# Kernel tuning notes

Measured on AMD Instinct MI355X. Metric: run time of the kernel, lower is better.

## Reference

```python
import jax, jax.numpy as jnp
import numpy as np

N_HEADS, N_LEVELS, N_POINTS = 8, 4, 4


def _bilinear(im, grid, H, W):
    # im: [N, D, H*W] flattened level feature, grid: [N, Q, P, 2] in [-1, 1]
    # F.grid_sample bilinear, padding_mode='zeros', align_corners=False
    N, Q, P, _ = grid.shape
    D = im.shape[1]
    gx = ((grid[..., 0] + 1.0) * W - 1.0) * 0.5
    gy = ((grid[..., 1] + 1.0) * H - 1.0) * 0.5
    x0f = jnp.floor(gx)
    y0f = jnp.floor(gy)
    x0 = x0f.astype(jnp.int32)
    y0 = y0f.astype(jnp.int32)
    wx1 = gx - x0f
    wy1 = gy - y0f
    acc = jnp.zeros((N, D, Q * P), im.dtype)
    corners = ((0, 0, (1 - wx1) * (1 - wy1)), (1, 0, wx1 * (1 - wy1)),
               (0, 1, (1 - wx1) * wy1), (1, 1, wx1 * wy1))
    for dx, dy, wgt in corners:
        xi = x0 + dx
        yi = y0 + dy
        valid = (xi >= 0) & (xi < W) & (yi >= 0) & (yi < H)
        idx = jnp.clip(yi, 0, H - 1) * W + jnp.clip(xi, 0, W - 1)
        v = jnp.take_along_axis(im, idx.reshape(N, 1, Q * P), axis=2)  # [N,D,QP]
        acc = acc + v * jnp.where(valid, wgt, 0.0).reshape(N, 1, Q * P)
    return acc.reshape(N, D, Q, P)


def _forward(query, value, reference_points, shapes_np,
             w_off, b_off, w_attn, b_attn, w_val, b_val, w_out, b_out):
    B, Q, E = query.shape
    H_, L, P = N_HEADS, N_LEVELS, N_POINTS
    D = E // H_
    v = (value @ w_val + b_val).reshape(B, -1, H_, D)  # [B, Nv, H, D]
    off = (query @ w_off + b_off).reshape(B, Q, H_, L, P, 2)
    attn = (query @ w_attn + b_attn).reshape(B, Q, H_, L * P)
    attn = jax.nn.softmax(attn, axis=-1).reshape(B, Q, H_, L, P)
    # offset_scale = [W_l, H_l] per level
    scale = jnp.asarray(np.stack([shapes_np[:, 1], shapes_np[:, 0]], -1), jnp.float32)
    locs = reference_points[:, :, None, :, None, :] + off / scale[None, None, None, :, None, :]
    grid = 2.0 * locs - 1.0  # [B, Q, H, L, P, 2]
    starts = np.concatenate([[0], np.cumsum(shapes_np[:, 0] * shapes_np[:, 1])]).astype(int)
    out = jnp.zeros((B * H_, D, Q), query.dtype)
    for lvl in range(L):
        h, w = int(shapes_np[lvl, 0]), int(shapes_np[lvl, 1])
        feat = v[:, starts[lvl]:starts[lvl + 1]]                      # [B, h*w, H, D]
        feat = feat.transpose(0, 2, 3, 1).reshape(B * H_, D, h * w)   # [BH, D, hw]
        g = jnp.transpose(grid[:, :, :, lvl], (0, 2, 1, 3, 4)).reshape(B * H_, Q, P, 2)
        sampled = _bilinear(feat, g, h, w)                            # [BH, D, Q, P]
        wl = jnp.transpose(attn[:, :, :, lvl], (0, 2, 1, 3)).reshape(B * H_, 1, Q, P)
        out = out + (sampled * wl).sum(-1)                            # [BH, D, Q]
    out = out.reshape(B, H_ * D, Q).transpose(0, 2, 1)                # [B, Q, E]
    return out @ w_out + b_out


def setup_inputs() -> dict:
    key = jax.random.key(0)
    ks = jax.random.split(key, 12)
    B, Q, E = 2, 19947, 256
    L, H_, P = N_LEVELS, N_HEADS, N_POINTS
    shapes = jnp.array([[100, 150], [50, 75], [25, 38], [13, 19]], dtype=jnp.int64)
    s = 0.02
    return {
        'query': jax.random.normal(ks[0], (B, Q, E), jnp.float32),
        'value': jax.random.normal(ks[1], (B, Q, E), jnp.float32),
        'reference_points': jax.random.uniform(ks[2], (B, Q, L, 2), jnp.float32),
        'spatial_shapes': shapes,
        'w_off': jax.random.normal(ks[3], (E, H_ * L * P * 2), jnp.float32) * s,
        'b_off': jax.random.normal(ks[4], (H_ * L * P * 2,), jnp.float32) * s,
        'w_attn': jax.random.normal(ks[5], (E, H_ * L * P), jnp.float32) * s,
        'b_attn': jax.random.normal(ks[6], (H_ * L * P,), jnp.float32) * s,
        'w_val': jax.random.normal(ks[7], (E, E), jnp.float32) * s,
        'b_val': jax.random.normal(ks[8], (E,), jnp.float32) * s,
        'w_out': jax.random.normal(ks[9], (E, E), jnp.float32) * s,
        'b_out': jax.random.normal(ks[10], (E,), jnp.float32) * s,
    }


def reference(query, value, reference_points, spatial_shapes,
              w_off, b_off, w_attn, b_attn, w_val, b_val, w_out, b_out):
    shapes_np = np.asarray(spatial_shapes)
    return _forward(query, value, reference_points, shapes_np,
                    w_off, b_off, w_attn, b_attn, w_val, b_val, w_out, b_out)
```

## Files before the change

kernel.cpp:

```cpp
#include <hip/hip_runtime.h>
#include <math.h>

#define B_    2
#define Q_    19947
#define E_    256
#define H_    8
#define D_    32
#define L_    4
#define P_    4

typedef _Float16 f16_t;
typedef f16_t f16x8 __attribute__((ext_vector_type(8)));
typedef f16_t f16x4 __attribute__((ext_vector_type(4)));
typedef float f32x4 __attribute__((ext_vector_type(4)));

__global__ __launch_bounds__(256)
void transpose_all(const float* __restrict__ w_val, const float* __restrict__ w_off,
                   const float* __restrict__ w_attn, const float* __restrict__ w_out,
                   f16_t* __restrict__ WtV, f16_t* __restrict__ WtQ,
                   f16_t* __restrict__ WtO)
{
    const float* in; f16_t* out; int N;
    switch (blockIdx.z) {
        case 0:  in = w_val;  out = WtV;             N = 256; break;
        case 1:  in = w_off;  out = WtQ;             N = 256; break;
        case 2:  in = w_attn; out = WtQ + 256 * 256; N = 128; break;
        default: in = w_out;  out = WtO;             N = 256; break;
    }
    const int nt = blockIdx.x * 32;
    if (nt >= N) return;
    const int kt = blockIdx.y * 32;

    __shared__ float tile[32][33];
    const int x  = threadIdx.x & 31;
    const int y0 = threadIdx.x >> 5;
    #pragma unroll
    for (int p = 0; p < 4; ++p)
        tile[y0 + p * 8][x] = in[(size_t)(kt + y0 + p * 8) * N + nt + x];
    __syncthreads();
    #pragma unroll
    for (int p = 0; p < 4; ++p)
        out[(size_t)(nt + y0 + p * 8) * 256 + kt + x] = (f16_t)tile[x][y0 + p * 8];
}

__global__ __launch_bounds__(256, 5)
void gemm_proj(const float* __restrict__ Aval, const float* __restrict__ Aqry,
               const f16_t* __restrict__ WtV, const f16_t* __restrict__ WtQ,
               const float* __restrict__ b_val, const float* __restrict__ b_off,
               const float* __restrict__ b_attn,
               f16_t* __restrict__ v_proj, float* __restrict__ off_b,
               float* __restrict__ attn_b, int M)
{
    constexpr int K = 256, BK = 32, NIT = K / BK;
    __shared__ __align__(16) f16_t As[2][64][40];
    __shared__ __align__(16) f16_t Bs[2][128][40];

    const int t    = threadIdx.x;
    const int m0   = blockIdx.x * 64;
    const int by   = blockIdx.y;
    const bool isVal = (by < 2);
    const float*  Af = isVal ? Aval : Aqry;
    const f16_t*  Wt = isVal ? WtV : WtQ;
    const int n0     = isVal ? by * 128 : (by - 2) * 128;

    const int lane = t & 63;
    const int w    = t >> 6;
    const int wm   = w & 1, wn = w >> 1;
    const int quad = lane >> 4, l16 = lane & 15;

    const int srow = t >> 2;
    const int skc  = (t & 3) * 8;

    f32x4 acc[2][4];
    #pragma unroll
    for (int i = 0; i < 2; ++i)
        #pragma unroll
        for (int j = 0; j < 4; ++j) {
            f32x4 z = {0.f, 0.f, 0.f, 0.f};
            acc[i][j] = z;
        }

    f16x8 aval;
    uint4 bval0, bval1;

    auto load_stage = [&](int k0) {
        const int gm = m0 + srow;
        if (gm < M) {
            const float4 v0 = *(const float4*)(Af + (size_t)gm * 256 + k0 + skc);
            const float4 v1 = *(const float4*)(Af + (size_t)gm * 256 + k0 + skc + 4);
            aval[0] = (f16_t)v0.x; aval[1] = (f16_t)v0.y;
            aval[2] = (f16_t)v0.z; aval[3] = (f16_t)v0.w;
            aval[4] = (f16_t)v1.x; aval[5] = (f16_t)v1.y;
            aval[6] = (f16_t)v1.z; aval[7] = (f16_t)v1.w;
        } else {
            #pragma unroll
            for (int i = 0; i < 8; ++i) aval[i] = (f16_t)0.f;
        }
        bval0 = *(const uint4*)(Wt + (size_t)(n0 + srow)      * 256 + k0 + skc);
        bval1 = *(const uint4*)(Wt + (size_t)(n0 + srow + 64) * 256 + k0 + skc);
    };
    auto store_stage = [&](int buf) {
        *(f16x8*)&As[buf][srow][skc]      = aval;
        *(uint4*)&Bs[buf][srow][skc]      = bval0;
        *(uint4*)&Bs[buf][srow + 64][skc] = bval1;
    };

    load_stage(0);
    store_stage(0);
    int cur = 0;

    #pragma unroll
    for (int it = 0; it < NIT; ++it) {
        __syncthreads();
        if (it + 1 < NIT)
            load_stage((it + 1) * BK);

        f16x8 af[2], bfr[4];
        #pragma unroll
        for (int i = 0; i < 2; ++i)
            af[i] = *(const f16x8*)&As[cur][wm * 32 + i * 16 + l16][quad * 8];
        #pragma unroll
        for (int j = 0; j < 4; ++j)
            bfr[j] = *(const f16x8*)&Bs[cur][wn * 64 + j * 16 + l16][quad * 8];
        #pragma unroll
        for (int i = 0; i < 2; ++i)
            #pragma unroll
            for (int j = 0; j < 4; ++j)
                acc[i][j] = __builtin_amdgcn_mfma_f32_16x16x32_f16(af[i], bfr[j], acc[i][j], 0, 0, 0);

        if (it + 1 < NIT)
            store_stage(cur ^ 1);
        cur ^= 1;
    }

    #pragma unroll
    for (int j = 0; j < 4; ++j) {
        const int gn = n0 + wn * 64 + j * 16 + l16;
        const float bv = isVal ? b_val[gn] : (gn < 256 ? b_off[gn] : b_attn[gn - 256]);
        #pragma unroll
        for (int i = 0; i < 2; ++i) {
            #pragma unroll
            for (int r = 0; r < 4; ++r) {
                const int gm = m0 + wm * 32 + i * 16 + quad * 4 + r;
                if (gm < M) {
                    const float val = acc[i][j][r] + bv;
                    if (isVal)
                        v_proj[(size_t)gm * 256 + gn] = (f16_t)val;
                    else if (gn < 256)
                        off_b[(size_t)gm * 256 + gn] = val;
                    else
                        attn_b[(size_t)gm * 128 + (gn - 256)] = val;
                }
            }
        }
    }
}

__global__ __launch_bounds__(256, 4)
void msda_fused(const f16_t* __restrict__ v,
                const float* __restrict__ off,
                const float* __restrict__ attn,
                const float* __restrict__ ref,
                const f16_t* __restrict__ WoT,
                const float* __restrict__ b_out,
                float* __restrict__ out,
                int BQ)
{
    constexpr int SH[4] = {100, 50, 25, 13};
    constexpr int SW[4] = {150, 75, 38, 19};
    constexpr int ST[4] = {0, 15000, 18750, 19700};

    __shared__ __align__(16) f16_t Samp[16][264];

    const int t   = threadIdx.x;
    const int bq0 = blockIdx.x * 16;

    #pragma unroll
    for (int r = 0; r < 2; ++r) {
        const int g    = t >> 2;
        const int qi   = (g >> 3) + r * 8;
        const int h    = g & 7;
        const int lane = t & 3;
        const int bq   = bq0 + qi;

        float acc[8] = {0.f, 0.f, 0.f, 0.f, 0.f, 0.f, 0.f, 0.f};

        if (bq < BQ) {
            const int b = bq / Q_;
            const f16_t* vbase = v + ((size_t)b * Q_) * E_ + h * D_ + lane * 8;
            const float* offp  = off  + (size_t)bq * 256 + h * 32;
            const float* attnp = attn + (size_t)bq * 128 + h * 16;

            float aw[16];
            #pragma unroll
            for (int i = 0; i < 4; ++i) {
                const float4 x = *(const float4*)(attnp + i * 4);
                aw[i*4+0] = x.x; aw[i*4+1] = x.y; aw[i*4+2] = x.z; aw[i*4+3] = x.w;
            }
            float mx = aw[0];
            #pragma unroll
            for (int i = 1; i < 16; ++i) mx = fmaxf(mx, aw[i]);
            float sum = 0.f;
            #pragma unroll
            for (int i = 0; i < 16; ++i) { aw[i] = expf(aw[i] - mx); sum += aw[i]; }
            const float inv = 1.f / sum;
            #pragma unroll
            for (int i = 0; i < 16; ++i) aw[i] *= inv;

            const float4 r01 = *(const float4*)(ref + (size_t)bq * 8);
            const float4 r23 = *(const float4*)(ref + (size_t)bq * 8 + 4);
            const float rx[4] = {r01.x, r01.z, r23.x, r23.z};
            const float ry[4] = {r01.y, r01.w, r23.y, r23.w};

            #pragma unroll
            for (int l = 0; l < L_; ++l) {
                const float fW = (float)SW[l], fH = (float)SH[l];
                const int   Ww = SW[l], Hh = SH[l], st = ST[l];
                #pragma unroll
                for (int pp = 0; pp < 2; ++pp) {
                    const float4 o2 = *(const float4*)(offp + l * 8 + pp * 4);
                    #pragma unroll
                    for (int q = 0; q < 2; ++q) {
                        const int   p  = pp * 2 + q;
                        const float ox = q ? o2.z : o2.x;
                        const float oy = q ? o2.w : o2.y;
                        const float wA = aw[l * 4 + p];
                        const float gx = fmaf(rx[l], fW, ox) - 0.5f;
                        const float gy = fmaf(ry[l], fH, oy) - 0.5f;
                        const float x0f = floorf(gx), y0f = floorf(gy);
                        const int   x0  = (int)x0f,   y0  = (int)y0f;
                        const float wx1 = gx - x0f,   wy1 = gy - y0f;
                        const float wx0 = 1.f - wx1,  wy0 = 1.f - wy1;

                        const float mxw0 = ((unsigned)x0     < (unsigned)Ww) ? wx0 : 0.f;
                        const float mxw1 = ((unsigned)(x0+1) < (unsigned)Ww) ? wx1 : 0.f;
                        const float myw0 = ((unsigned)y0     < (unsigned)Hh) ? wy0 : 0.f;
                        const float myw1 = ((unsigned)(y0+1) < (unsigned)Hh) ? wy1 : 0.f;
                        const int xc0 = min(max(x0, 0),     Ww - 1);
                        const int xc1 = min(max(x0 + 1, 0), Ww - 1);
                        const int yc0 = min(max(y0, 0),     Hh - 1);
                        const int yc1 = min(max(y0 + 1, 0), Hh - 1);

                        const float w00 = wA * mxw0 * myw0;
                        const float w10 = wA * mxw1 * myw0;
                        const float w01 = wA * mxw0 * myw1;
                        const float w11 = wA * mxw1 * myw1;

                        const f16x8 s00 = *(const f16x8*)(vbase + (size_t)(st + yc0 * Ww + xc0) * E_);
                        const f16x8 s10 = *(const f16x8*)(vbase + (size_t)(st + yc0 * Ww + xc1) * E_);
                        const f16x8 s01 = *(const f16x8*)(vbase + (size_t)(st + yc1 * Ww + xc0) * E_);
                        const f16x8 s11 = *(const f16x8*)(vbase + (size_t)(st + yc1 * Ww + xc1) * E_);

                        #pragma unroll
                        for (int c = 0; c < 8; ++c) {
                            acc[c] = fmaf(w00, (float)s00[c], acc[c]);
                            acc[c] = fmaf(w10, (float)s10[c], acc[c]);
                            acc[c] = fmaf(w01, (float)s01[c], acc[c]);
                            acc[c] = fmaf(w11, (float)s11[c], acc[c]);
                        }
                    }
                }
            }
        }

        f16x8 o;
        #pragma unroll
        for (int c = 0; c < 8; ++c) o[c] = (f16_t)acc[c];
        *(f16x8*)&Samp[qi][h * 32 + lane * 8] = o;
    }

    __syncthreads();

    const int lane = t & 63;
    const int w    = t >> 6;
    const int quad = lane >> 4, l16 = lane & 15;

    f16x8 af[8];
    #pragma unroll
    for (int kf = 0; kf < 8; ++kf)
        af[kf] = *(const f16x8*)&Samp[l16][kf * 32 + quad * 8];

    f32x4 acc4[4];
    #pragma unroll
    for (int j = 0; j < 4; ++j) {
        f32x4 z = {0.f, 0.f, 0.f, 0.f};
        acc4[j] = z;
    }

    #pragma unroll
    for (int j = 0; j < 4; ++j) {
        const int n = w * 64 + j * 16 + l16;
        const f16_t* bp = WoT + (size_t)n * 256 + quad * 8;
        #pragma unroll
        for (int kf = 0; kf < 8; ++kf) {
            const f16x8 bfr = *(const f16x8*)(bp + kf * 32);
            acc4[j] = __builtin_amdgcn_mfma_f32_16x16x32_f16(af[kf], bfr, acc4[j], 0, 0, 0);
        }
    }

    #pragma unroll
    for (int j = 0; j < 4; ++j) {
        const int n  = w * 64 + j * 16 + l16;
        const float bv = b_out[n];
        #pragma unroll
        for (int r = 0; r < 4; ++r) {
            const int gm = bq0 + quad * 4 + r;
            if (gm < BQ)
                out[(size_t)gm * 256 + n] = acc4[j][r] + bv;
        }
    }
}

extern "C" void kernel_launch(void* const* d_in, const int* in_sizes, int n_in,
                              void* d_out, int out_size, void* d_ws, size_t ws_size,
                              hipStream_t stream)
{
    const float* query  = (const float*)d_in[0];
    const float* value  = (const float*)d_in[1];
    const float* refpts = (const float*)d_in[2];
    const float* w_off  = (const float*)d_in[4];
    const float* b_off  = (const float*)d_in[5];
    const float* w_attn = (const float*)d_in[6];
    const float* b_attn = (const float*)d_in[7];
    const float* w_val  = (const float*)d_in[8];
    const float* b_val  = (const float*)d_in[9];
    const float* w_out  = (const float*)d_in[10];
    const float* b_out  = (const float*)d_in[11];
    float* out = (float*)d_out;

    const int BQ = B_ * Q_;

    char* ws = (char*)d_ws;
    f16_t* v_proj = (f16_t*)ws;                       ws += (size_t)BQ * 256 * 2;
    float* off_b  = (float*)ws;                       ws += (size_t)BQ * 256 * 4;
    float* attn_b = (float*)ws;                       ws += (size_t)BQ * 128 * 4;
    f16_t* WtV    = (f16_t*)ws;                       ws += (size_t)256 * 256 * 2;
    f16_t* WtQ    = (f16_t*)ws;                       ws += (size_t)384 * 256 * 2;
    f16_t* WtO    = (f16_t*)ws;

    const dim3 blk(256);

    transpose_all<<<dim3(8, 8, 4), blk, 0, stream>>>(w_val, w_off, w_attn, w_out,
                                                     WtV, WtQ, WtO);

    const int mg = (BQ + 63) / 64;

    gemm_proj<<<dim3(mg, 5), blk, 0, stream>>>(
        value, query, WtV, WtQ, b_val, b_off, b_attn,
        v_proj, off_b, attn_b, BQ);

    msda_fused<<<dim3((BQ + 15) / 16), blk, 0, stream>>>(
        v_proj, off_b, attn_b, refpts, WtO, b_out, out, BQ);
}
```

Measured before the change: 297.2 us.

## Replace LDS-staged projection GEMM with direct-to-register MFMA operand loads

```diff
diff --git a/kernel.cpp b/kernel.cpp
--- a/kernel.cpp
+++ b/kernel.cpp
@@ -43,33 +43,37 @@
         out[(size_t)(nt + y0 + p * 8) * 256 + kt + x] = (f16_t)tile[x][y0 + p * 8];
 }
 
-__global__ __launch_bounds__(256, 5)
-void gemm_proj(const float* __restrict__ Aval, const float* __restrict__ Aqry,
-               const f16_t* __restrict__ WtV, const f16_t* __restrict__ WtQ,
-               const float* __restrict__ b_val, const float* __restrict__ b_off,
-               const float* __restrict__ b_attn,
-               f16_t* __restrict__ v_proj, float* __restrict__ off_b,
-               float* __restrict__ attn_b, int M)
+__global__ __launch_bounds__(256)
+void gemm_direct(const float* __restrict__ value, const float* __restrict__ query,
+                 const f16_t* __restrict__ WtV, const f16_t* __restrict__ WtQ,
+                 const float* __restrict__ b_val, const float* __restrict__ b_off,
+                 const float* __restrict__ b_attn,
+                 f16_t* __restrict__ v_proj, float* __restrict__ off_b,
+                 float* __restrict__ attn_b, int M)
 {
-    constexpr int K = 256, BK = 32, NIT = K / BK;
-    __shared__ __align__(16) f16_t As[2][64][40];
-    __shared__ __align__(16) f16_t Bs[2][128][40];
-
     const int t    = threadIdx.x;
-    const int m0   = blockIdx.x * 64;
-    const int by   = blockIdx.y;
-    const bool isVal = (by < 2);
-    const float*  Af = isVal ? Aval : Aqry;
-    const f16_t*  Wt = isVal ? WtV : WtQ;
-    const int n0     = isVal ? by * 128 : (by - 2) * 128;
-
+    const int w    = t >> 6;
     const int lane = t & 63;
-    const int w    = t >> 6;
-    const int wm   = w & 1, wn = w >> 1;
     const int quad = lane >> 4, l16 = lane & 15;
 
-    const int srow = t >> 2;
-    const int skc  = (t & 3) * 8;
+    const int by     = blockIdx.y;
+    const bool isVal = (by < 4);
+    const float* A   = isVal ? value : query;
+    const f16_t* Wt  = isVal ? WtV : WtQ;
+    const int n0     = isVal ? by * 64 : (by - 4) * 64;
+
+    const int mb = blockIdx.x * 128 + w * 32;
+
+    const float* aptr[2];
+    #pragma unroll
+    for (int i = 0; i < 2; ++i) {
+        const int gm = min(mb + i * 16 + l16, M - 1);
+        aptr[i] = A + (size_t)gm * 256 + quad * 8;
+    }
+    const f16_t* bptr[4];
+    #pragma unroll
+    for (int j = 0; j < 4; ++j)
+        bptr[j] = Wt + (size_t)(n0 + j * 16 + l16) * 256 + quad * 8;
 
     f32x4 acc[2][4];
     #pragma unroll
@@ -80,68 +84,68 @@
             acc[i][j] = z;
         }
 
-    f16x8 aval;
-    uint4 bval0, bval1;
-
-    auto load_stage = [&](int k0) {
-        const int gm = m0 + srow;
-        if (gm < M) {
-            const float4 v0 = *(const float4*)(Af + (size_t)gm * 256 + k0 + skc);
-            const float4 v1 = *(const float4*)(Af + (size_t)gm * 256 + k0 + skc + 4);
-            aval[0] = (f16_t)v0.x; aval[1] = (f16_t)v0.y;
-            aval[2] = (f16_t)v0.z; aval[3] = (f16_t)v0.w;
-            aval[4] = (f16_t)v1.x; aval[5] = (f16_t)v1.y;
-            aval[6] = (f16_t)v1.z; aval[7] = (f16_t)v1.w;
-        } else {
-            #pragma unroll
-            for (int i = 0; i < 8; ++i) aval[i] = (f16_t)0.f;
-        }
-        bval0 = *(const uint4*)(Wt + (size_t)(n0 + srow)      * 256 + k0 + skc);
-        bval1 = *(const uint4*)(Wt + (size_t)(n0 + srow + 64) * 256 + k0 + skc);
-    };
-    auto store_stage = [&](int buf) {
-        *(f16x8*)&As[buf][srow][skc]      = aval;
-        *(uint4*)&Bs[buf][srow][skc]      = bval0;
-        *(uint4*)&Bs[buf][srow + 64][skc] = bval1;
-    };
-
-    load_stage(0);
-    store_stage(0);
-    int cur = 0;
-
-    #pragma unroll
-    for (int it = 0; it < NIT; ++it) {
-        __syncthreads();
-        if (it + 1 < NIT)
-            load_stage((it + 1) * BK);
-
-        f16x8 af[2], bfr[4];
+    float4 acur[2][2], anxt[2][2];
+    uint4  bcur[4],    bnxt[4];
+
+    #pragma unroll
+    for (int i = 0; i < 2; ++i) {
+        acur[i][0] = *(const float4*)(aptr[i]);
+        acur[i][1] = *(const float4*)(aptr[i] + 4);
+    }
+    #pragma unroll
+    for (int j = 0; j < 4; ++j)
+        bcur[j] = *(const uint4*)(bptr[j]);
+
+    #pragma unroll
+    for (int it = 0; it < 8; ++it) {
+        if (it < 7) {
+            const int k1 = (it + 1) * 32;
+            #pragma unroll
+            for (int i = 0; i < 2; ++i) {
+                anxt[i][0] = *(const float4*)(aptr[i] + k1);
+                anxt[i][1] = *(const float4*)(aptr[i] + k1 + 4);
+            }
+            #pragma unroll
+            for (int j = 0; j < 4; ++j)
+                bnxt[j] = *(const uint4*)(bptr[j] + k1);
+        }
+
+        f16x8 af[2];
+        #pragma unroll
+        for (int i = 0; i < 2; ++i) {
+            af[i][0] = (f16_t)acur[i][0].x; af[i][1] = (f16_t)acur[i][0].y;
+            af[i][2] = (f16_t)acur[i][0].z; af[i][3] = (f16_t)acur[i][0].w;
+            af[i][4] = (f16_t)acur[i][1].x; af[i][5] = (f16_t)acur[i][1].y;
+            af[i][6] = (f16_t)acur[i][1].z; af[i][7] = (f16_t)acur[i][1].w;
+        }
         #pragma unroll
         for (int i = 0; i < 2; ++i)
-            af[i] = *(const f16x8*)&As[cur][wm * 32 + i * 16 + l16][quad * 8];
-        #pragma unroll
-        for (int j = 0; j < 4; ++j)
-            bfr[j] = *(const f16x8*)&Bs[cur][wn * 64 + j * 16 + l16][quad * 8];
-        #pragma unroll
-        for (int i = 0; i < 2; ++i)
             #pragma unroll
             for (int j = 0; j < 4; ++j)
-                acc[i][j] = __builtin_amdgcn_mfma_f32_16x16x32_f16(af[i], bfr[j], acc[i][j], 0, 0, 0);
-
-        if (it + 1 < NIT)
-            store_stage(cur ^ 1);
-        cur ^= 1;
+                acc[i][j] = __builtin_amdgcn_mfma_f32_16x16x32_f16(
+                    af[i], *(const f16x8*)&bcur[j], acc[i][j], 0, 0, 0);
+
+        if (it < 7) {
+            #pragma unroll
+            for (int i = 0; i < 2; ++i) {
+                acur[i][0] = anxt[i][0];
+                acur[i][1] = anxt[i][1];
+            }
+            #pragma unroll
+            for (int j = 0; j < 4; ++j)
+                bcur[j] = bnxt[j];
+        }
     }
 
     #pragma unroll
     for (int j = 0; j < 4; ++j) {
-        const int gn = n0 + wn * 64 + j * 16 + l16;
+        const int gn = n0 + j * 16 + l16;
         const float bv = isVal ? b_val[gn] : (gn < 256 ? b_off[gn] : b_attn[gn - 256]);
         #pragma unroll
         for (int i = 0; i < 2; ++i) {
             #pragma unroll
             for (int r = 0; r < 4; ++r) {
-                const int gm = m0 + wm * 32 + i * 16 + quad * 4 + r;
+                const int gm = mb + i * 16 + quad * 4 + r;
                 if (gm < M) {
                     const float val = acc[i][j][r] + bv;
                     if (isVal)
@@ -343,9 +347,7 @@
     transpose_all<<<dim3(8, 8, 4), blk, 0, stream>>>(w_val, w_off, w_attn, w_out,
                                                      WtV, WtQ, WtO);
 
-    const int mg = (BQ + 63) / 64;
-
-    gemm_proj<<<dim3(mg, 5), blk, 0, stream>>>(
+    gemm_direct<<<dim3((BQ + 127) / 128, 10), blk, 0, stream>>>(
         value, query, WtV, WtQ, b_val, b_off, b_attn,
         v_proj, off_b, attn_b, BQ);
 
```

After: 350.9 us. +18.1%, slower.
